# Optimization experiments

Hardware: AMD Instinct MI355X
Metric: run time of the kernel (lower is better)

Reference implementation:

```python
import jax, jax.numpy as jnp
import numpy as np

DIM = 4096
N_HEADS = 32
N_KV_HEADS = 8
HEAD_DIM = DIM // N_HEADS  # 128
B, S = 1, 2048
ROPE_THETA = 10000.0


def setup_inputs() -> dict:
    key = jax.random.key(0)
    kx, kq, kk, kv, ko = jax.random.split(key, 5)
    x = jax.random.normal(kx, (B, S, DIM), dtype=jnp.float32)
    # torch Linear weights are [out_features, in_features]
    wq = jax.random.normal(kq, (N_HEADS * HEAD_DIM, DIM), dtype=jnp.float32) * 0.02
    wk = jax.random.normal(kk, (N_KV_HEADS * HEAD_DIM, DIM), dtype=jnp.float32) * 0.02
    wv = jax.random.normal(kv, (N_KV_HEADS * HEAD_DIM, DIM), dtype=jnp.float32) * 0.02
    wo = jax.random.normal(ko, (DIM, N_HEADS * HEAD_DIM), dtype=jnp.float32) * 0.02
    # RoPE table [S, HEAD_DIM, 2]; frequencies repeated twice to match the
    # even/odd interleaved rotate_half convention of apply_rope.
    pos = jnp.arange(S, dtype=jnp.float32)
    inv_freq = 1.0 / (ROPE_THETA ** (jnp.arange(0, HEAD_DIM, 2, dtype=jnp.float32) / HEAD_DIM))
    ang = pos[:, None] * inv_freq[None, :]          # [S, HEAD_DIM/2]
    ang = jnp.repeat(ang, 2, axis=-1)               # [S, HEAD_DIM]
    rope_freqs = jnp.stack([jnp.cos(ang), jnp.sin(ang)], axis=-1)  # [S, HEAD_DIM, 2]
    return {"x": x, "wq": wq, "wk": wk, "wv": wv, "wo": wo,
            "rope_freqs": rope_freqs, "start_pos": 0}


def _rotate_half(t):
    # interleaved: (x0,x1,x2,x3,...) -> (-x1,x0,-x3,x2,...)
    t1 = t[..., ::2]
    t2 = t[..., 1::2]
    return jnp.stack((-t2, t1), axis=-1).reshape(t.shape)


def reference(x, wq, wk, wv, wo, rope_freqs, start_pos):
    b, s, _ = x.shape
    rep = N_HEADS // N_KV_HEADS
    scale = 1.0 / np.sqrt(HEAD_DIM)

    q = (x @ wq.T).reshape(b, s, N_HEADS, HEAD_DIM)
    k = (x @ wk.T).reshape(b, s, N_KV_HEADS, HEAD_DIM)
    v = (x @ wv.T).reshape(b, s, N_KV_HEADS, HEAD_DIM)

    cos = rope_freqs[..., 0][None, :, None, :]  # [1,S,1,HEAD_DIM]
    sin = rope_freqs[..., 1][None, :, None, :]
    q = q * cos + _rotate_half(q) * sin
    k = k * cos + _rotate_half(k) * sin

    # GQA without materializing repeated K/V: group query heads by kv head.
    qg = q.reshape(b, s, N_KV_HEADS, rep, HEAD_DIM)
    scores = jnp.einsum("bsgrd,btgd->bgrst", qg, k) * scale  # [B,KV,rep,S,S]
    causal = jnp.tril(jnp.ones((s, s), dtype=bool))
    scores = jnp.where(causal, scores, jnp.finfo(scores.dtype).min)
    attn = jax.nn.softmax(scores, axis=-1)
    out = jnp.einsum("bgrst,btgd->bsgrd", attn, v)           # [B,S,KV,rep,HEAD_DIM]
    out = out.reshape(b, s, N_HEADS * HEAD_DIM)
    return out @ wo.T
```

## Files before the change

kernel.cpp:

```cpp
#include <hip/hip_runtime.h>
#include <stdint.h>

#define DIM 4096
#define NH 32
#define NKV 8
#define HD 128
#define SEQ 2048
#define KVD 1024

typedef unsigned short u16;
typedef __attribute__((ext_vector_type(8))) short bf16x8;
typedef __attribute__((ext_vector_type(4))) float f32x4;

__device__ __forceinline__ float bf2f(u16 v){
  union { unsigned u; float f; } c; c.u = ((unsigned)v) << 16; return c.f;
}
__device__ __forceinline__ u16 f2bf(float f){
  union { float f; unsigned u; } c; c.f = f;
  unsigned u = c.u;
  u += 0x7FFF + ((u >> 16) & 1);
  return (u16)(u >> 16);
}
__device__ __forceinline__ unsigned pack2bf(float a, float b){
  return (unsigned)f2bf(a) | ((unsigned)f2bf(b) << 16);
}

__device__ __forceinline__ void gl_lds16(const void* g, void* l){
  __builtin_amdgcn_global_load_lds((const __attribute__((address_space(1))) void*)g,
                                   (__attribute__((address_space(3))) void*)l, 16, 0, 0);
}

#define VM3 asm volatile("s_waitcnt vmcnt(3)" ::: "memory")
#define VM2 asm volatile("s_waitcnt vmcnt(2)" ::: "memory")
#define VM0 asm volatile("s_waitcnt vmcnt(0)" ::: "memory")
#define LGKM0 asm volatile("s_waitcnt lgkmcnt(0)" ::: "memory")
#define SB0 __builtin_amdgcn_sched_barrier(0)
#define BAR __builtin_amdgcn_s_barrier()

__global__ void cvt_all(const float* __restrict__ x,  const float* __restrict__ wq,
                        const float* __restrict__ wk, const float* __restrict__ wv,
                        const float* __restrict__ wo,
                        u16* __restrict__ xb,  u16* __restrict__ wqb,
                        u16* __restrict__ wkb, u16* __restrict__ wvb,
                        u16* __restrict__ wob){
  const int b = blockIdx.x;
  const float* in; u16* out; int base;
  if      (b <  8192){ in = x;  out = xb;  base = b; }
  else if (b < 24576){ in = wq; out = wqb; base = b - 8192; }
  else if (b < 28672){ in = wk; out = wkb; base = b - 24576; }
  else if (b < 32768){ in = wv; out = wvb; base = b - 28672; }
  else               { in = wo; out = wob; base = b - 32768; }
  const int i = (base*256 + threadIdx.x)*4;
  float4 v = *(const float4*)(in + i);
  ushort4 o;
  o.x = f2bf(v.x); o.y = f2bf(v.y); o.z = f2bf(v.z); o.w = f2bf(v.w);
  *(ushort4*)(out + i) = o;
}

__global__ void add_f32(float* __restrict__ out, const float* __restrict__ p){
  const int i = blockIdx.x*256 + threadIdx.x;
  float4 a = ((const float4*)out)[i];
  const float4 b = ((const float4*)p)[i];
  a.x += b.x; a.y += b.y; a.z += b.z; a.w += b.w;
  ((float4*)out)[i] = a;
}

template<int BUNITS, int EPI>
__global__ __launch_bounds__(512, 2) void gemmP(const u16* __restrict__ A,
    const u16* __restrict__ B, void* __restrict__ C0, void* __restrict__ C1,
    void* __restrict__ C2, const float* __restrict__ rf, float* __restrict__ Cp){
  constexpr int BN = BUNITS*64;
  __shared__ __align__(16) char lds[65536 + BUNITS*16384];
  const int t = threadIdx.x, w = t >> 6, l = t & 63;
  const int lg = l >> 4, li = l & 15;
  const int wr = w >> 2, wc = w & 3;
  const int idx = ((int)blockIdx.x & 7)*32 + ((int)blockIdx.x >> 3);

  int bm, bn, kbase, nt, ks = 0;
  if (EPI == 0){ bm = idx & 7; bn = idx >> 3; kbase = 0; nt = 64; }
  else         { bm = idx & 7; ks = (idx >> 3) & 1; bn = idx >> 4; kbase = ks*2048; nt = 32; }
  const u16* Ab = A + (size_t)bm*256*DIM;
  const u16* Bb = B + (size_t)bn*BN*DIM;

  auto stA = [&](int k0, int abase, int u){
    const int r = u*64 + (t >> 3);
    gl_lds16(Ab + (size_t)r*DIM + k0 + (((t & 7) ^ (r & 7)) << 3),
             lds + abase + u*8192 + (t >> 3)*128 + (t & 7)*16);
  };
  auto stB = [&](int k0, int bbase, int u){
    const int r = u*64 + (t >> 3);
    gl_lds16(Bb + (size_t)r*DIM + k0 + (((t & 7) ^ (r & 7)) << 3),
             lds + bbase + u*8192 + (t >> 3)*128 + (t & 7)*16);
  };

  f32x4 acc[8][BUNITS] = {};
  bf16x8 bfr[BUNITS][2];

#define PH(p, ...) { \
    bf16x8 af[2][2]; \
    _Pragma("unroll") \
    for (int q = 0; q < 2; ++q){ \
      const int R = wr*128 + (2*(p)+q)*16 + li; \
      af[q][0] = *(const bf16x8*)(ldsA + R*128 + (( lg    ^ (R & 7)) << 4)); \
      af[q][1] = *(const bf16x8*)(ldsA + R*128 + (((lg+4) ^ (R & 7)) << 4)); \
    } \
    if ((p) == 0){ \
      _Pragma("unroll") \
      for (int j = 0; j < BUNITS; ++j){ \
        const int R = wc*(BUNITS*16) + j*16 + li; \
        bfr[j][0] = *(const bf16x8*)(ldsB + R*128 + (( lg    ^ (R & 7)) << 4)); \
        bfr[j][1] = *(const bf16x8*)(ldsB + R*128 + (((lg+4) ^ (R & 7)) << 4)); \
      } \
    } \
    __VA_ARGS__; \
    BAR; LGKM0; SB0; \
    __builtin_amdgcn_s_setprio(1); \
    _Pragma("unroll") \
    for (int q = 0; q < 2; ++q) \
      _Pragma("unroll") \
      for (int j = 0; j < BUNITS; ++j){ \
        acc[2*(p)+q][j] = __builtin_amdgcn_mfma_f32_16x16x32_bf16(af[q][0], bfr[j][0], acc[2*(p)+q][j], 0, 0, 0); \
        acc[2*(p)+q][j] = __builtin_amdgcn_mfma_f32_16x16x32_bf16(af[q][1], bfr[j][1], acc[2*(p)+q][j], 0, 0, 0); \
      } \
    __builtin_amdgcn_s_setprio(0); \
    BAR; }

  #pragma unroll
  for (int u = 0; u < BUNITS; ++u) stB(kbase, 65536, u);
  stA(kbase, 0, 0); stA(kbase, 0, 2);
  stA(kbase, 0, 1); stA(kbase, 0, 3);
  VM2; BAR;

  for (int tt = 0; tt < nt; ++tt){
    const int buf = tt & 1, b2 = buf ^ 1;
    const int k1 = kbase + (tt+1)*64;
    const bool pf = (tt + 1 < nt);
    const char* ldsA = lds + buf*32768;
    const char* ldsB = lds + 65536 + buf*BUNITS*8192;
    const int a2 = b2*32768, b2o = 65536 + b2*BUNITS*8192;

    PH(0, if (pf){ stB(k1, b2o, 0); stB(k1, b2o, 1); stB(k1, b2o, 2); })
    PH(1, if (pf){ VM3; if constexpr (BUNITS == 4) stB(k1, b2o, 3);
                   stA(k1, a2, 0); stA(k1, a2, 2); }
          else   { VM0; })
    PH(2, if (pf){ stA(k1, a2, 1); })
    PH(3, if (pf){ stA(k1, a2, 3); VM2; })
  }
#undef PH

  if (EPI == 1){
    float* C = (float*)(ks ? Cp : C0);
    #pragma unroll
    for (int i = 0; i < 8; ++i){
      const int srow = bm*256 + wr*128 + i*16 + lg*4;
      #pragma unroll
      for (int j = 0; j < BUNITS; ++j){
        const int col = bn*BN + wc*(BUNITS*16) + j*16 + li;
        #pragma unroll
        for (int r = 0; r < 4; ++r)
          C[(size_t)(srow + r)*DIM + col] = acc[i][j][r];
      }
    }
  } else {
    #pragma unroll
    for (int i = 0; i < 8; ++i){
      const int srow0 = bm*256 + wr*128 + i*16 + lg*4;
      #pragma unroll
      for (int j = 0; j < BUNITS; ++j){
        const int fc0 = bn*BN + wc*(BUNITS*16) + j*16;
        const int col = fc0 + li;
        if (fc0 < 5120){
          u16* C  = (fc0 < 4096) ? (u16*)C0 : (u16*)C1;
          const int ldc  = (fc0 < 4096) ? DIM : KVD;
          const int ccol = (fc0 < 4096) ? col : col - 4096;
          const int i4 = ((col & 127) >> 1) << 2;
          #pragma unroll
          for (int r = 0; r < 4; ++r){
            const float v = acc[i][j][r];
            const float p = __shfl_xor(v, 1);
            const int srow = srow0 + r;
            const float cs = rf[(size_t)srow*256 + i4];
            const float sn = rf[(size_t)srow*256 + i4 + 1];
            const float o = (col & 1) ? (v*cs + p*sn) : (v*cs - p*sn);
            C[(size_t)srow*ldc + ccol] = f2bf(o);
          }
        } else {
          u16* C = (u16*)C2;
          ushort4 o;
          o.x = f2bf(acc[i][j][0]); o.y = f2bf(acc[i][j][1]);
          o.z = f2bf(acc[i][j][2]); o.w = f2bf(acc[i][j][3]);
          *(ushort4*)&C[(size_t)(col - 5120)*SEQ + srow0] = o;
        }
      }
    }
  }
}

__global__ __launch_bounds__(256) void flash_attn(const u16* __restrict__ Q,
                                                  const u16* __restrict__ Kg,
                                                  const u16* __restrict__ Vt,
                                                  u16* __restrict__ O){
  __shared__ bf16x8 smK[2][64*16];
  __shared__ bf16x8 smV[2][128*8];
  __shared__ __align__(16) u16 smP[4][16*64];
  const int bid = blockIdx.x;
  const int h  = bid & 31;
  const int qt = 31 - (bid >> 5);
  const int g  = h >> 2;
  const int t = threadIdx.x, w = t >> 6, l = t & 63;
  const int lg = l >> 4, li = l & 15;

  bf16x8 qf[4];
  {
    const u16* qrow = Q + (size_t)(qt*64 + w*16 + li)*DIM + h*HD;
    #pragma unroll
    for (int kc = 0; kc < 4; ++kc)
      qf[kc] = *(const bf16x8*)(qrow + kc*32 + lg*8);
  }
  f32x4 accO[8] = {};
  float mrun = -1e30f, lsum = 0.f;
  const float SC = 0.08838834764831845f * 1.4426950408889634f;

  const int ksrow = t >> 4, ksslot = t & 15;
  const int vsrow = t >> 3, vsslot = t & 7;

  auto stage = [&](int kt, int b){
    #pragma unroll
    for (int j = 0; j < 4; ++j){
      const int krow = j*16 + ksrow;
      const int ksl = (ksslot & 8) | ((ksslot ^ (krow & 7)) & 7);
      gl_lds16(Kg + (size_t)(kt*64 + krow)*KVD + g*HD + ksl*8, (char*)&smK[b][0] + j*4096 + w*1024);
      const int vrow = j*32 + vsrow;
      const int vsl = (vsslot ^ (vrow & 7)) & 7;
      gl_lds16(Vt + (size_t)(g*HD + vrow)*SEQ + kt*64 + vsl*8, (char*)&smV[b][0] + j*4096 + w*1024);
    }
  };

  stage(0, 0);
  int buf = 0;
  u16* pw = &smP[w][0];

  for (int kt = 0; kt <= qt; ++kt){
    __syncthreads();
    if (kt < qt) stage(kt + 1, buf ^ 1);

    f32x4 sacc[4] = {};
    __builtin_amdgcn_s_setprio(1);
    #pragma unroll
    for (int kc = 0; kc < 4; ++kc){
      #pragma unroll
      for (int nj = 0; nj < 4; ++nj){
        const int R = nj*16 + li;
        int sl = lg + 4*kc;
        sl = (sl & 8) | ((sl ^ (R & 7)) & 7);
        sacc[nj] = __builtin_amdgcn_mfma_f32_16x16x32_bf16(smK[buf][R*16 + sl], qf[kc], sacc[nj], 0, 0, 0);
      }
    }
    __builtin_amdgcn_s_setprio(0);
    float p[4][4];
    #pragma unroll
    for (int nj = 0; nj < 4; ++nj)
      #pragma unroll
      for (int r = 0; r < 4; ++r)
        p[nj][r] = sacc[nj][r] * SC;
    if (kt == qt){
      const int qloc = w*16 + li;
      #pragma unroll
      for (int nj = 0; nj < 4; ++nj)
        #pragma unroll
        for (int r = 0; r < 4; ++r)
          if (nj*16 + lg*4 + r > qloc) p[nj][r] = -1e30f;
    }
    float mx = p[0][0];
    #pragma unroll
    for (int nj = 0; nj < 4; ++nj)
      #pragma unroll
      for (int r = 0; r < 4; ++r) mx = fmaxf(mx, p[nj][r]);
    mx = fmaxf(mx, __shfl_xor(mx, 16));
    mx = fmaxf(mx, __shfl_xor(mx, 32));
    if (!__all(mx - mrun <= 8.f)){
      const float mnew = fmaxf(mrun, mx);
      const float alpha = exp2f(mrun - mnew);
      lsum *= alpha;
      float al[4];
      #pragma unroll
      for (int r = 0; r < 4; ++r) al[r] = __shfl(alpha, (l & 48) | (lg*4 + r));
      #pragma unroll
      for (int dj = 0; dj < 8; ++dj)
        #pragma unroll
        for (int r = 0; r < 4; ++r) accO[dj][r] *= al[r];
      mrun = mnew;
    }
    float s = 0.f;
    #pragma unroll
    for (int nj = 0; nj < 4; ++nj)
      #pragma unroll
      for (int r = 0; r < 4; ++r){ p[nj][r] = exp2f(p[nj][r] - mrun); s += p[nj][r]; }
    s += __shfl_xor(s, 16);
    s += __shfl_xor(s, 32);
    lsum += s;
    #pragma unroll
    for (int nj = 0; nj < 4; ++nj){
      const int c = nj*2 + (lg >> 1);
      uint2 v; v.x = pack2bf(p[nj][0], p[nj][1]); v.y = pack2bf(p[nj][2], p[nj][3]);
      *(uint2*)((char*)pw + li*128 + ((c ^ (li & 7)) << 4) + ((lg & 1) << 3)) = v;
    }
    __builtin_amdgcn_s_setprio(1);
    #pragma unroll
    for (int kc2 = 0; kc2 < 2; ++kc2){
      const bf16x8 pf = *(const bf16x8*)((char*)pw + li*128 + (((kc2*4 + lg) ^ (li & 7)) << 4));
      #pragma unroll
      for (int dj = 0; dj < 8; ++dj){
        const int R = dj*16 + li;
        const bf16x8 vf = smV[buf][R*8 + ((lg + 4*kc2) ^ (R & 7))];
        accO[dj] = __builtin_amdgcn_mfma_f32_16x16x32_bf16(pf, vf, accO[dj], 0, 0, 0);
      }
    }
    __builtin_amdgcn_s_setprio(0);
    buf ^= 1;
  }
  float linv[4];
  #pragma unroll
  for (int r = 0; r < 4; ++r) linv[r] = 1.f / __shfl(lsum, (l & 48) | (lg*4 + r));
  #pragma unroll
  for (int dj = 0; dj < 8; ++dj)
    #pragma unroll
    for (int r = 0; r < 4; ++r)
      O[(size_t)(qt*64 + w*16 + lg*4 + r)*DIM + h*HD + dj*16 + li] = f2bf(accO[dj][r] * linv[r]);
}

extern "C" void kernel_launch(void* const* d_in, const int* in_sizes, int n_in,
                              void* d_out, int out_size, void* d_ws, size_t ws_size,
                              hipStream_t stream){
  const float* x  = (const float*)d_in[0];
  const float* wq = (const float*)d_in[1];
  const float* wk = (const float*)d_in[2];
  const float* wv = (const float*)d_in[3];
  const float* wo = (const float*)d_in[4];
  const float* rf = (const float*)d_in[5];
  float* out = (float*)d_out;

  char* ws = (char*)d_ws;
  size_t off = 0;
  auto alloc = [&](size_t nbytes){ void* p = ws + off; off += (nbytes + 255) & ~(size_t)255; return p; };
  u16* xb  = (u16*)alloc((size_t)SEQ*DIM*2);
  u16* wqb = (u16*)alloc((size_t)DIM*DIM*2);
  u16* wkb = (u16*)alloc((size_t)KVD*DIM*2);
  u16* wvb = (u16*)alloc((size_t)KVD*DIM*2);
  u16* wob = (u16*)alloc((size_t)DIM*DIM*2);
  u16* Qb  = (u16*)alloc((size_t)SEQ*DIM*2);
  u16* K8  = (u16*)alloc((size_t)SEQ*KVD*2);
  u16* Vtr = (u16*)alloc((size_t)KVD*SEQ*2);
  u16* AO  = (u16*)alloc((size_t)SEQ*DIM*2);
  float* P1 = (float*)wqb;

  cvt_all<<<49152, 256, 0, stream>>>(x, wq, wk, wv, wo, xb, wqb, wkb, wvb, wob);

  gemmP<3, 0><<<256, 512, 0, stream>>>(xb, wqb, Qb, K8, Vtr, rf, nullptr);

  flash_attn<<<SEQ/64 * NH, 256, 0, stream>>>(Qb, K8, Vtr, AO);

  gemmP<4, 1><<<256, 512, 0, stream>>>(AO, wob, out, nullptr, nullptr, nullptr, P1);
  add_f32<<<8192, 256, 0, stream>>>(out, P1);
}
```

Baseline: 305.4 us.

## Deepen GEMM global-to-LDS prefetch to two tiles ahead with split stores

Restructures the GEMM main loop so that B tiles and half of the A tiles are prefetched two k-steps ahead, while the remaining A halves are loaded one step ahead, all using the existing double-buffered LDS. The vmcnt waits are retuned (VM7/8/10/12) to match the larger number of in-flight loads. The intent is to hide global memory latency better by keeping more loads outstanding. It relies on correct buffer reuse ordering: B and the A halves for tile tt+2 are written into the current buffer after its reads in earlier phases, so a wrong wait count or missing barrier would cause races.

```diff
diff --git a/kernel.cpp b/kernel.cpp
--- a/kernel.cpp
+++ b/kernel.cpp
@@ -30,9 +30,12 @@
                                    (__attribute__((address_space(3))) void*)l, 16, 0, 0);
 }
 
-#define VM3 asm volatile("s_waitcnt vmcnt(3)" ::: "memory")
-#define VM2 asm volatile("s_waitcnt vmcnt(2)" ::: "memory")
-#define VM0 asm volatile("s_waitcnt vmcnt(0)" ::: "memory")
+#define VM0  asm volatile("s_waitcnt vmcnt(0)"  ::: "memory")
+#define VM2  asm volatile("s_waitcnt vmcnt(2)"  ::: "memory")
+#define VM7  asm volatile("s_waitcnt vmcnt(7)"  ::: "memory")
+#define VM8  asm volatile("s_waitcnt vmcnt(8)"  ::: "memory")
+#define VM10 asm volatile("s_waitcnt vmcnt(10)" ::: "memory")
+#define VM12 asm volatile("s_waitcnt vmcnt(12)" ::: "memory")
 #define LGKM0 asm volatile("s_waitcnt lgkmcnt(0)" ::: "memory")
 #define SB0 __builtin_amdgcn_sched_barrier(0)
 #define BAR __builtin_amdgcn_s_barrier()
@@ -129,22 +132,31 @@
   for (int u = 0; u < BUNITS; ++u) stB(kbase, 65536, u);
   stA(kbase, 0, 0); stA(kbase, 0, 2);
   stA(kbase, 0, 1); stA(kbase, 0, 3);
-  VM2; BAR;
+  #pragma unroll
+  for (int u = 0; u < BUNITS; ++u) stB(kbase + 64, 65536 + BUNITS*8192, u);
+  stA(kbase + 64, 32768, 0); stA(kbase + 64, 32768, 2);
+  if constexpr (BUNITS == 3) VM7; else VM8;
+  BAR;
 
   for (int tt = 0; tt < nt; ++tt){
-    const int buf = tt & 1, b2 = buf ^ 1;
-    const int k1 = kbase + (tt+1)*64;
-    const bool pf = (tt + 1 < nt);
-    const char* ldsA = lds + buf*32768;
-    const char* ldsB = lds + 65536 + buf*BUNITS*8192;
-    const int a2 = b2*32768, b2o = 65536 + b2*BUNITS*8192;
-
-    PH(0, if (pf){ stB(k1, b2o, 0); stB(k1, b2o, 1); stB(k1, b2o, 2); })
-    PH(1, if (pf){ VM3; if constexpr (BUNITS == 4) stB(k1, b2o, 3);
-                   stA(k1, a2, 0); stA(k1, a2, 2); }
-          else   { VM0; })
-    PH(2, if (pf){ stA(k1, a2, 1); })
-    PH(3, if (pf){ stA(k1, a2, 3); VM2; })
+    const int k1 = kbase + (tt+1)*64, k2 = kbase + (tt+2)*64;
+    const char* ldsA = lds + (tt & 1)*32768;
+    const char* ldsB = lds + 65536 + (tt & 1)*BUNITS*8192;
+    const int aCur = (tt & 1)*32768;
+    const int aNxt = ((tt+1) & 1)*32768;
+    const int bCur = 65536 + (tt & 1)*BUNITS*8192;
+
+    PH(0, if (tt+1 < nt){ stA(k1, aNxt, 1); stA(k1, aNxt, 3); })
+    PH(1, if (tt+2 < nt){ _Pragma("unroll")
+                          for (int u = 0; u < BUNITS; ++u) stB(k2, bCur, u); }
+          if (tt == nt-1){ VM0; }
+          else if (tt == nt-2){ if constexpr (BUNITS == 3) VM7; else VM8; }
+          else { if constexpr (BUNITS == 3) VM10; else VM12; } )
+    PH(2, if (tt+2 < nt){ stA(k2, aCur, 0); stA(k2, aCur, 2); })
+    PH(3, if (tt+1 < nt){
+            if (tt+1 == nt-1){ VM2; }
+            else { if constexpr (BUNITS == 3) VM7; else VM8; }
+          } )
   }
 #undef PH
 
```

New measurement: 305.7 us. Within noise of the previous version (+0.1%).
